# Performance work log

Hardware: AMD Instinct MI355X
Metric: run time of the kernel (lower is better)

## Reference

```python
import jax, jax.numpy as jnp
import numpy as np

B, S, H, I, E, TOPK = 2, 2048, 1024, 2048, 8, 2


def setup_inputs() -> dict:
    key = jax.random.key(0)
    ks = jax.random.split(key, 6)
    return {
        "x": jax.random.normal(ks[0], (B, S, H), dtype=jnp.float32),
        "expert_indices": jax.random.randint(ks[1], (B, S, TOPK), 0, E, dtype=jnp.int64),
        "expert_weights": jax.random.uniform(ks[2], (B, S, TOPK), dtype=jnp.float32),
        "gate_proj": jax.random.normal(ks[3], (E, I, H), dtype=jnp.float32) * 0.02,
        "up_proj": jax.random.normal(ks[4], (E, I, H), dtype=jnp.float32) * 0.02,
        "down_proj": jax.random.normal(ks[5], (E, H, I), dtype=jnp.float32) * 0.02,
    }


def reference(x, expert_indices, expert_weights, gate_proj, up_proj, down_proj):
    # x: [B,S,H]; expert_indices/weights: [B,S,K]; gate/up: [E,I,H]; down: [E,H,I]
    b, s, h = x.shape
    e = gate_proj.shape[0]
    xf = x.reshape(-1, h)                      # [T,H]
    t = xf.shape[0]
    idx = expert_indices.reshape(t, -1)        # [T,K]
    w = expert_weights.reshape(t, -1)          # [T,K]
    # Combine per-(token,slot) weights into a per-(token,expert) weight matrix.
    # Identical math to the per-expert index_add_ in the torch module.
    we = jnp.zeros((t, e), dtype=x.dtype).at[jnp.arange(t)[:, None], idx].add(w)  # [T,E]
    gate = jax.nn.silu(jnp.einsum('th,eih->tei', xf, gate_proj))  # [T,E,I]
    up = jnp.einsum('th,eih->tei', xf, up_proj)                   # [T,E,I]
    out_e = jnp.einsum('tei,ehi->teh', gate * up, down_proj)      # [T,E,H]
    out = jnp.einsum('te,teh->th', we, out_e)                     # [T,H]
    return out.reshape(b, s, h)
```

## Files before the change

kernel.cpp:

```cpp
#include <hip/hip_runtime.h>


#define H_DIM 1024
#define I_DIM 2048
#define N_EXP 8
#define N_TOK 4096
#define N_ENT 8192
#define CAP   9216

typedef __attribute__((ext_vector_type(8))) short bhalf8;
typedef __attribute__((ext_vector_type(4))) float floatx4;

__device__ __forceinline__ unsigned short f2bf(float f) {
  unsigned int u = __float_as_uint(f);
  u += 0x7fffu + ((u >> 16) & 1u);
  return (unsigned short)(u >> 16);
}

__device__ __forceinline__ unsigned int pkbf(float a, float b) {
  unsigned int ua = __float_as_uint(a) + 0x8000u;
  unsigned int ub = __float_as_uint(b) + 0x8000u;
  return __builtin_amdgcn_perm(ub, ua, 0x07060302u);
}

__device__ __forceinline__ void ld16(const void* g, void* l) {
  __builtin_amdgcn_global_load_lds(
      (const __attribute__((address_space(1))) unsigned int*)g,
      (__attribute__((address_space(3))) unsigned int*)l, 16, 0, 0);
}

__global__ __launch_bounds__(256) void prep_kernel(
    const float* __restrict__ x, unsigned short* __restrict__ xb,
    const int* __restrict__ idx, const float* __restrict__ wts,
    int* __restrict__ perm, float* __restrict__ pw, int* __restrict__ inv,
    int* __restrict__ counts, int* __restrict__ poff)
{
  __shared__ int cnt[N_EXP], cur[N_EXP], off[N_EXP];
  const int t = threadIdx.x;
  if (blockIdx.x < (N_TOK * H_DIM) / (256 * 8)) {
    size_t i = ((size_t)blockIdx.x * 256 + t) * 8;
    const float4* sp = (const float4*)(x + i);
    float4 a = sp[0], b = sp[1];
    bhalf8 o;
    o[0] = (short)f2bf(a.x); o[1] = (short)f2bf(a.y); o[2] = (short)f2bf(a.z); o[3] = (short)f2bf(a.w);
    o[4] = (short)f2bf(b.x); o[5] = (short)f2bf(b.y); o[6] = (short)f2bf(b.z); o[7] = (short)f2bf(b.w);
    *(bhalf8*)(xb + i) = o;
    return;
  }
  if (t < N_EXP) { cnt[t] = 0; cur[t] = 0; }
  __syncthreads();
  for (int i = t; i < N_ENT; i += 256) atomicAdd(&cnt[idx[i] & 7], 1);
  __syncthreads();
  if (t == 0) {
    int o = 0;
    for (int e = 0; e < N_EXP; e++) {
      off[e] = o; counts[e] = cnt[e]; poff[e] = o;
      o += ((cnt[e] + 127) >> 7) << 7;
    }
  }
  __syncthreads();
  for (int i = t; i < N_ENT; i += 256) {
    int e = idx[i] & 7;
    int p = atomicAdd(&cur[e], 1);
    int pos = off[e] + p;
    perm[pos] = i >> 1;
    pw[pos] = wts[i];
    inv[i] = pos;
  }
}

__global__ __launch_bounds__(512, 4) void gemm1_kernel(
    const unsigned short* __restrict__ xb,
    const float* __restrict__ gw,
    const float* __restrict__ uw,
    const int* __restrict__ perm,
    const int* __restrict__ counts,
    const int* __restrict__ poff,
    unsigned short* __restrict__ act)
{
  const int e = blockIdx.z;
  const int Ne = counts[e];
  const int mt = blockIdx.y;
  if (mt * 256 >= Ne) return;
  const int NeR = ((Ne + 127) >> 7) << 7;
  const int base = poff[e];
  const int n0 = blockIdx.x * 64;

  __shared__ __align__(16) unsigned short As[256 * 64];
  __shared__ __align__(16) unsigned short Bgs[64 * 64];
  __shared__ __align__(16) unsigned short Bus[64 * 64];

  const int tid = threadIdx.x;
  const int lane = tid & 63;
  const int w = tid >> 6;
  const int wmi = w >> 1;
  const int wnj = w & 1;
  const int i3 = lane >> 3, i7 = lane & 7;
  const int swc = (i7 ^ i3) * 8;

  const unsigned short* pA[4]; unsigned short* lA[4];
#pragma unroll
  for (int t = 0; t < 4; t++) {
    int rloc = w * 32 + t * 8 + i3;
    int rr = mt * 256 + rloc; rr = rr < Ne ? rr : Ne - 1;
    pA[t] = xb + (size_t)perm[base + rr] * H_DIM + swc;
    lA[t] = &As[(w * 32 + t * 8) * 64];
  }
  const int nlocB = w * 8 + i3;
  const size_t wb = (size_t)e * (I_DIM * H_DIM) + (size_t)(n0 + nlocB) * H_DIM + i7 * 8;
  const float* pg = gw + wb;
  const float* pu = uw + wb;
  unsigned short* lBg = &Bgs[nlocB * 64 + ((i7 ^ i3) * 8)];
  unsigned short* lBu = &Bus[nlocB * 64 + ((i7 ^ i3) * 8)];

  floatx4 zero = {0.f, 0.f, 0.f, 0.f};
  floatx4 accg[4][2], accu[4][2];
#pragma unroll
  for (int i = 0; i < 4; i++)
#pragma unroll
    for (int j = 0; j < 2; j++) { accg[i][j] = zero; accu[i][j] = zero; }

  const int quad = lane >> 4, lm = lane & 15;
  const int s7 = lm & 7;

  float4 g0 = *(const float4*)(pg);
  float4 g1 = *(const float4*)(pg + 4);
  float4 u0 = *(const float4*)(pu);
  float4 u1 = *(const float4*)(pu + 4);

  for (int k0 = 0; k0 < H_DIM; k0 += 64) {
    __syncthreads();
#pragma unroll
    for (int t = 0; t < 4; t++) ld16(pA[t] + k0, lA[t]);
    *(uint4*)lBg = make_uint4(pkbf(g0.x, g0.y), pkbf(g0.z, g0.w),
                              pkbf(g1.x, g1.y), pkbf(g1.z, g1.w));
    *(uint4*)lBu = make_uint4(pkbf(u0.x, u0.y), pkbf(u0.z, u0.w),
                              pkbf(u1.x, u1.y), pkbf(u1.z, u1.w));
    __syncthreads();
    if (k0 + 64 < H_DIM) {
      g0 = *(const float4*)(pg + k0 + 64);
      g1 = *(const float4*)(pg + k0 + 68);
      u0 = *(const float4*)(pu + k0 + 64);
      u1 = *(const float4*)(pu + k0 + 68);
    }
#pragma unroll
    for (int kk = 0; kk < 2; kk++) {
      const int kq = kk * 4 + quad;
      const int ko = (kq ^ s7) * 8;
      bhalf8 a[4], bg[2], bu[2];
#pragma unroll
      for (int i = 0; i < 4; i++)
        a[i] = *(const bhalf8*)&As[(wmi * 64 + i * 16 + lm) * 64 + ko];
#pragma unroll
      for (int j = 0; j < 2; j++) {
        bg[j] = *(const bhalf8*)&Bgs[(wnj * 32 + j * 16 + lm) * 64 + ko];
        bu[j] = *(const bhalf8*)&Bus[(wnj * 32 + j * 16 + lm) * 64 + ko];
      }
#pragma unroll
      for (int i = 0; i < 4; i++)
#pragma unroll
        for (int j = 0; j < 2; j++) {
          accg[i][j] = __builtin_amdgcn_mfma_f32_16x16x32_bf16(a[i], bg[j], accg[i][j], 0, 0, 0);
          accu[i][j] = __builtin_amdgcn_mfma_f32_16x16x32_bf16(a[i], bu[j], accu[i][j], 0, 0, 0);
        }
    }
  }

#pragma unroll
  for (int i = 0; i < 4; i++) {
#pragma unroll
    for (int r = 0; r < 4; r++) {
      int row = mt * 256 + wmi * 64 + i * 16 + quad * 4 + r;
      if (row < NeR) {
        size_t rowoff = (size_t)(base + row) * I_DIM;
#pragma unroll
        for (int j = 0; j < 2; j++) {
          int col = n0 + wnj * 32 + j * 16 + lm;
          float g = accg[i][j][r];
          float u = accu[i][j][r];
          float h = (g / (1.f + __expf(-g))) * u;
          act[rowoff + col] = (unsigned short)f2bf(h);
        }
      }
    }
  }
}

__global__ __launch_bounds__(512, 4) void gemm2_kernel(
    const unsigned short* __restrict__ act,
    const float* __restrict__ dw,
    const float* __restrict__ pw,
    const int* __restrict__ counts,
    const int* __restrict__ poff,
    float* __restrict__ ent)
{
  const int e = blockIdx.z;
  const int Ne = counts[e];
  const int mt = blockIdx.y;
  if (mt * 256 >= Ne) return;
  const int NeR = ((Ne + 127) >> 7) << 7;
  const int base = poff[e];
  const int n0 = (blockIdx.x & 7) * 128;
  const int k_lo = (blockIdx.x >> 3) * (I_DIM / 2);

  __shared__ __align__(16) unsigned short As[256 * 64];
  __shared__ __align__(16) unsigned short Bs[128 * 64];

  const int tid = threadIdx.x;
  const int lane = tid & 63;
  const int w = tid >> 6;
  const int wmi = w >> 1, wnj = w & 1;
  const int i3 = lane >> 3, i7 = lane & 7;
  const int swc = (i7 ^ i3) * 8;

  const unsigned short* pA[4]; unsigned short* lA[4];
#pragma unroll
  for (int t = 0; t < 4; t++) {
    int rloc = w * 32 + t * 8 + i3;
    int rr = mt * 256 + rloc; rr = rr < NeR ? rr : NeR - 1;
    pA[t] = act + (size_t)(base + rr) * I_DIM + k_lo + swc;
    lA[t] = &As[(w * 32 + t * 8) * 64];
  }
  const float* pB[2]; unsigned short* lB[2];
#pragma unroll
  for (int t = 0; t < 2; t++) {
    int rloc = w * 16 + t * 8 + i3;
    pB[t] = dw + (size_t)e * (H_DIM * I_DIM) + (size_t)(n0 + rloc) * I_DIM + k_lo + i7 * 8;
    lB[t] = &Bs[rloc * 64 + ((i7 ^ i3) * 8)];
  }

  floatx4 zero = {0.f, 0.f, 0.f, 0.f};
  floatx4 acc[4][4];
#pragma unroll
  for (int i = 0; i < 4; i++)
#pragma unroll
    for (int j = 0; j < 4; j++) acc[i][j] = zero;

  const int quad = lane >> 4, lm = lane & 15;
  const int s7 = lm & 7;

  float4 b00 = *(const float4*)(pB[0]);
  float4 b01 = *(const float4*)(pB[0] + 4);
  float4 b10 = *(const float4*)(pB[1]);
  float4 b11 = *(const float4*)(pB[1] + 4);

  for (int k0 = 0; k0 < I_DIM / 2; k0 += 64) {
    __syncthreads();
#pragma unroll
    for (int t = 0; t < 4; t++) ld16(pA[t] + k0, lA[t]);
    *(uint4*)lB[0] = make_uint4(pkbf(b00.x, b00.y), pkbf(b00.z, b00.w),
                                pkbf(b01.x, b01.y), pkbf(b01.z, b01.w));
    *(uint4*)lB[1] = make_uint4(pkbf(b10.x, b10.y), pkbf(b10.z, b10.w),
                                pkbf(b11.x, b11.y), pkbf(b11.z, b11.w));
    __syncthreads();
    if (k0 + 64 < I_DIM / 2) {
      b00 = *(const float4*)(pB[0] + k0 + 64);
      b01 = *(const float4*)(pB[0] + k0 + 68);
      b10 = *(const float4*)(pB[1] + k0 + 64);
      b11 = *(const float4*)(pB[1] + k0 + 68);
    }
#pragma unroll
    for (int kk = 0; kk < 2; kk++) {
      const int kq = kk * 4 + quad;
      const int ko = (kq ^ s7) * 8;
      bhalf8 a[4], b[4];
#pragma unroll
      for (int i = 0; i < 4; i++)
        a[i] = *(const bhalf8*)&As[(wmi * 64 + i * 16 + lm) * 64 + ko];
#pragma unroll
      for (int j = 0; j < 4; j++)
        b[j] = *(const bhalf8*)&Bs[(wnj * 64 + j * 16 + lm) * 64 + ko];
#pragma unroll
      for (int i = 0; i < 4; i++)
#pragma unroll
        for (int j = 0; j < 4; j++)
          acc[i][j] = __builtin_amdgcn_mfma_f32_16x16x32_bf16(a[i], b[j], acc[i][j], 0, 0, 0);
    }
  }

  float* enth = ent + (size_t)(blockIdx.x >> 3) * CAP * H_DIM;
#pragma unroll
  for (int i = 0; i < 4; i++) {
#pragma unroll
    for (int r = 0; r < 4; r++) {
      int row = mt * 256 + wmi * 64 + i * 16 + quad * 4 + r;
      if (row < Ne) {
        float wt = pw[base + row];
        float* orow = enth + (size_t)(base + row) * H_DIM;
#pragma unroll
        for (int j = 0; j < 4; j++) {
          int col = n0 + wnj * 64 + j * 16 + lm;
          orow[col] = wt * acc[i][j][r];
        }
      }
    }
  }
}

__global__ __launch_bounds__(256) void combine_kernel(
    const float* __restrict__ ent, const int* __restrict__ inv,
    float* __restrict__ out)
{
  const int t = blockIdx.x;
  const int p0 = inv[2 * t], p1 = inv[2 * t + 1];
  const float4* r0 = (const float4*)(ent + (size_t)p0 * H_DIM);
  const float4* r1 = (const float4*)(ent + (size_t)p1 * H_DIM);
  const float4* r2 = (const float4*)(ent + (size_t)(CAP + p0) * H_DIM);
  const float4* r3 = (const float4*)(ent + (size_t)(CAP + p1) * H_DIM);
  float4 a = r0[threadIdx.x], b = r1[threadIdx.x];
  float4 c = r2[threadIdx.x], d = r3[threadIdx.x];
  float4 o = {a.x + b.x + c.x + d.x, a.y + b.y + c.y + d.y,
              a.z + b.z + c.z + d.z, a.w + b.w + c.w + d.w};
  ((float4*)(out + (size_t)t * H_DIM))[threadIdx.x] = o;
}

extern "C" void kernel_launch(void* const* d_in, const int* in_sizes, int n_in,
                              void* d_out, int out_size, void* d_ws, size_t ws_size,
                              hipStream_t stream) {
  const float* x    = (const float*)d_in[0];
  const int*   idx  = (const int*)d_in[1];
  const float* wts  = (const float*)d_in[2];
  const float* gate = (const float*)d_in[3];
  const float* up   = (const float*)d_in[4];
  const float* down = (const float*)d_in[5];
  float* out = (float*)d_out;
  char* ws = (char*)d_ws;

  float*          ent = (float*)(ws + 0);
  unsigned short* act = (unsigned short*)(ws + 75497472);
  unsigned short* xb  = (unsigned short*)(ws + 113246208);
  int*   perm   = (int*)(ws + 121634816);
  float* pw     = (float*)(ws + 121671680);
  int*   inv    = (int*)(ws + 121708544);
  int*   counts = (int*)(ws + 121741312);
  int*   poff   = (int*)(ws + 121741376);

  prep_kernel<<<(N_TOK * H_DIM) / (256 * 8) + 1, 256, 0, stream>>>(
      x, xb, idx, wts, perm, pw, inv, counts, poff);

  gemm1_kernel<<<dim3(I_DIM / 64, 32, N_EXP), 512, 0, stream>>>(
      xb, gate, up, perm, counts, poff, act);

  gemm2_kernel<<<dim3(16, 32, N_EXP), 512, 0, stream>>>(
      act, down, pw, counts, poff, ent);

  combine_kernel<<<N_TOK, 256, 0, stream>>>(ent, inv, out);
}
```

Measured before the change: 383.9 us.

## Fuse combine into down-projection via atomic scatter-add into zeroed output

The output is zeroed inside the prep kernel. The down-projection GEMM then atomically adds weighted results directly into each token's output row using perm. This removes the large per-entry intermediate buffer, the inverse index array and the separate combine kernel. It relies on float atomics, which add L2 atomic traffic and make summation order nondeterministic.

```diff
diff --git a/kernel.cpp b/kernel.cpp
--- a/kernel.cpp
+++ b/kernel.cpp
@@ -31,8 +31,9 @@
 
 __global__ __launch_bounds__(256) void prep_kernel(
     const float* __restrict__ x, unsigned short* __restrict__ xb,
+    float* __restrict__ out,
     const int* __restrict__ idx, const float* __restrict__ wts,
-    int* __restrict__ perm, float* __restrict__ pw, int* __restrict__ inv,
+    int* __restrict__ perm, float* __restrict__ pw,
     int* __restrict__ counts, int* __restrict__ poff)
 {
   __shared__ int cnt[N_EXP], cur[N_EXP], off[N_EXP];
@@ -45,6 +46,10 @@
     o[0] = (short)f2bf(a.x); o[1] = (short)f2bf(a.y); o[2] = (short)f2bf(a.z); o[3] = (short)f2bf(a.w);
     o[4] = (short)f2bf(b.x); o[5] = (short)f2bf(b.y); o[6] = (short)f2bf(b.z); o[7] = (short)f2bf(b.w);
     *(bhalf8*)(xb + i) = o;
+    float4 z4 = {0.f, 0.f, 0.f, 0.f};
+    float4* op = (float4*)(out + (size_t)blockIdx.x * 2048);
+    op[t] = z4;
+    op[t + 256] = z4;
     return;
   }
   if (t < N_EXP) { cnt[t] = 0; cur[t] = 0; }
@@ -65,7 +70,6 @@
     int pos = off[e] + p;
     perm[pos] = i >> 1;
     pw[pos] = wts[i];
-    inv[i] = pos;
   }
 }
 
@@ -190,9 +194,10 @@
     const unsigned short* __restrict__ act,
     const float* __restrict__ dw,
     const float* __restrict__ pw,
+    const int* __restrict__ perm,
     const int* __restrict__ counts,
     const int* __restrict__ poff,
-    float* __restrict__ ent)
+    float* __restrict__ out)
 {
   const int e = blockIdx.z;
   const int Ne = counts[e];
@@ -278,7 +283,6 @@
     }
   }
 
-  float* enth = ent + (size_t)(blockIdx.x >> 3) * CAP * H_DIM;
 #pragma unroll
   for (int i = 0; i < 4; i++) {
 #pragma unroll
@@ -286,32 +290,15 @@
       int row = mt * 256 + wmi * 64 + i * 16 + quad * 4 + r;
       if (row < Ne) {
         float wt = pw[base + row];
-        float* orow = enth + (size_t)(base + row) * H_DIM;
+        float* orow = out + (size_t)perm[base + row] * H_DIM;
 #pragma unroll
         for (int j = 0; j < 4; j++) {
           int col = n0 + wnj * 64 + j * 16 + lm;
-          orow[col] = wt * acc[i][j][r];
+          atomicAdd(&orow[col], wt * acc[i][j][r]);
         }
       }
     }
   }
-}
-
-__global__ __launch_bounds__(256) void combine_kernel(
-    const float* __restrict__ ent, const int* __restrict__ inv,
-    float* __restrict__ out)
-{
-  const int t = blockIdx.x;
-  const int p0 = inv[2 * t], p1 = inv[2 * t + 1];
-  const float4* r0 = (const float4*)(ent + (size_t)p0 * H_DIM);
-  const float4* r1 = (const float4*)(ent + (size_t)p1 * H_DIM);
-  const float4* r2 = (const float4*)(ent + (size_t)(CAP + p0) * H_DIM);
-  const float4* r3 = (const float4*)(ent + (size_t)(CAP + p1) * H_DIM);
-  float4 a = r0[threadIdx.x], b = r1[threadIdx.x];
-  float4 c = r2[threadIdx.x], d = r3[threadIdx.x];
-  float4 o = {a.x + b.x + c.x + d.x, a.y + b.y + c.y + d.y,
-              a.z + b.z + c.z + d.z, a.w + b.w + c.w + d.w};
-  ((float4*)(out + (size_t)t * H_DIM))[threadIdx.x] = o;
 }
 
 extern "C" void kernel_launch(void* const* d_in, const int* in_sizes, int n_in,
@@ -326,23 +313,19 @@
   float* out = (float*)d_out;
   char* ws = (char*)d_ws;
 
-  float*          ent = (float*)(ws + 0);
-  unsigned short* act = (unsigned short*)(ws + 75497472);
-  unsigned short* xb  = (unsigned short*)(ws + 113246208);
-  int*   perm   = (int*)(ws + 121634816);
-  float* pw     = (float*)(ws + 121671680);
-  int*   inv    = (int*)(ws + 121708544);
-  int*   counts = (int*)(ws + 121741312);
-  int*   poff   = (int*)(ws + 121741376);
+  unsigned short* act = (unsigned short*)(ws + 0);
+  unsigned short* xb  = (unsigned short*)(ws + 37748736);
+  int*   perm   = (int*)(ws + 46137344);
+  float* pw     = (float*)(ws + 46174208);
+  int*   counts = (int*)(ws + 46211072);
+  int*   poff   = (int*)(ws + 46211136);
 
   prep_kernel<<<(N_TOK * H_DIM) / (256 * 8) + 1, 256, 0, stream>>>(
-      x, xb, idx, wts, perm, pw, inv, counts, poff);
+      x, xb, out, idx, wts, perm, pw, counts, poff);
 
   gemm1_kernel<<<dim3(I_DIM / 64, 32, N_EXP), 512, 0, stream>>>(
       xb, gate, up, perm, counts, poff, act);
 
   gemm2_kernel<<<dim3(16, 32, N_EXP), 512, 0, stream>>>(
-      act, down, pw, counts, poff, ent);
-
-  combine_kernel<<<N_TOK, 256, 0, stream>>>(ent, inv, out);
-}
+      act, down, pw, perm, counts, poff, out);
+}
```

Result: slower. 409.3 us (+6.6%).

## Double-buffer LDS tiles in both expert GEMM kernels to overlap loads with MFMA

Applied to the files above, without the earlier changes.

Both grouped GEMM kernels now keep two LDS buffers for the A and B tiles and alternate between them. The next K-slice is staged while the current one is computed, so each step needs one barrier instead of two. This is meant to hide global-load and LDS-write latency behind MFMA work. It doubles LDS use per block and lowers the occupancy hint in launch bounds from 4 to 2 blocks per CU, which can reduce latency hiding from concurrent blocks.

```diff
diff --git a/kernel.cpp b/kernel.cpp
--- a/kernel.cpp
+++ b/kernel.cpp
@@ -69,7 +69,44 @@
   }
 }
 
-__global__ __launch_bounds__(512, 4) void gemm1_kernel(
+#define G1_STAGE_A(ASX, KOFF)                                               \
+  _Pragma("unroll")                                                         \
+  for (int t_ = 0; t_ < 4; t_++) ld16(pA[t_] + (KOFF), &ASX[lAo[t_]]);
+
+#define G1_LOAD_B(KOFF)                                                     \
+  g0 = *(const float4*)(pg + (KOFF));  g1 = *(const float4*)(pg + (KOFF) + 4); \
+  u0 = *(const float4*)(pu + (KOFF));  u1 = *(const float4*)(pu + (KOFF) + 4);
+
+#define G1_WRITE_B(BGX, BUX)                                                \
+  *(uint4*)&BGX[bo] = make_uint4(pkbf(g0.x, g0.y), pkbf(g0.z, g0.w),        \
+                                 pkbf(g1.x, g1.y), pkbf(g1.z, g1.w));       \
+  *(uint4*)&BUX[bo] = make_uint4(pkbf(u0.x, u0.y), pkbf(u0.z, u0.w),        \
+                                 pkbf(u1.x, u1.y), pkbf(u1.z, u1.w));
+
+#define G1_COMPUTE(ASX, BGX, BUX)                                           \
+  _Pragma("unroll")                                                         \
+  for (int kk = 0; kk < 2; kk++) {                                          \
+    const int kq = kk * 4 + quad;                                           \
+    const int ko = (kq ^ s7) * 8;                                           \
+    bhalf8 a_[4], bg_[2], bu_[2];                                           \
+    _Pragma("unroll")                                                       \
+    for (int i = 0; i < 4; i++)                                             \
+      a_[i] = *(const bhalf8*)&ASX[(wmi * 64 + i * 16 + lm) * 64 + ko];     \
+    _Pragma("unroll")                                                       \
+    for (int j = 0; j < 2; j++) {                                           \
+      bg_[j] = *(const bhalf8*)&BGX[(wnj * 32 + j * 16 + lm) * 64 + ko];    \
+      bu_[j] = *(const bhalf8*)&BUX[(wnj * 32 + j * 16 + lm) * 64 + ko];    \
+    }                                                                       \
+    _Pragma("unroll")                                                       \
+    for (int i = 0; i < 4; i++)                                             \
+      _Pragma("unroll")                                                     \
+      for (int j = 0; j < 2; j++) {                                         \
+        accg[i][j] = __builtin_amdgcn_mfma_f32_16x16x32_bf16(a_[i], bg_[j], accg[i][j], 0, 0, 0); \
+        accu[i][j] = __builtin_amdgcn_mfma_f32_16x16x32_bf16(a_[i], bu_[j], accu[i][j], 0, 0, 0); \
+      }                                                                     \
+  }
+
+__global__ __launch_bounds__(512, 2) void gemm1_kernel(
     const unsigned short* __restrict__ xb,
     const float* __restrict__ gw,
     const float* __restrict__ uw,
@@ -86,9 +123,12 @@
   const int base = poff[e];
   const int n0 = blockIdx.x * 64;
 
-  __shared__ __align__(16) unsigned short As[256 * 64];
-  __shared__ __align__(16) unsigned short Bgs[64 * 64];
-  __shared__ __align__(16) unsigned short Bus[64 * 64];
+  __shared__ __align__(16) unsigned short As0[256 * 64];
+  __shared__ __align__(16) unsigned short As1[256 * 64];
+  __shared__ __align__(16) unsigned short Bg0[64 * 64];
+  __shared__ __align__(16) unsigned short Bg1[64 * 64];
+  __shared__ __align__(16) unsigned short Bu0[64 * 64];
+  __shared__ __align__(16) unsigned short Bu1[64 * 64];
 
   const int tid = threadIdx.x;
   const int lane = tid & 63;
@@ -98,20 +138,19 @@
   const int i3 = lane >> 3, i7 = lane & 7;
   const int swc = (i7 ^ i3) * 8;
 
-  const unsigned short* pA[4]; unsigned short* lA[4];
+  const unsigned short* pA[4]; int lAo[4];
 #pragma unroll
   for (int t = 0; t < 4; t++) {
     int rloc = w * 32 + t * 8 + i3;
     int rr = mt * 256 + rloc; rr = rr < Ne ? rr : Ne - 1;
     pA[t] = xb + (size_t)perm[base + rr] * H_DIM + swc;
-    lA[t] = &As[(w * 32 + t * 8) * 64];
+    lAo[t] = (w * 32 + t * 8) * 64;
   }
   const int nlocB = w * 8 + i3;
   const size_t wb = (size_t)e * (I_DIM * H_DIM) + (size_t)(n0 + nlocB) * H_DIM + i7 * 8;
   const float* pg = gw + wb;
   const float* pu = uw + wb;
-  unsigned short* lBg = &Bgs[nlocB * 64 + ((i7 ^ i3) * 8)];
-  unsigned short* lBu = &Bus[nlocB * 64 + ((i7 ^ i3) * 8)];
+  const int bo = nlocB * 64 + ((i7 ^ i3) * 8);
 
   floatx4 zero = {0.f, 0.f, 0.f, 0.f};
   floatx4 accg[4][2], accu[4][2];
@@ -123,48 +162,31 @@
   const int quad = lane >> 4, lm = lane & 15;
   const int s7 = lm & 7;
 
-  float4 g0 = *(const float4*)(pg);
-  float4 g1 = *(const float4*)(pg + 4);
-  float4 u0 = *(const float4*)(pu);
-  float4 u1 = *(const float4*)(pu + 4);
-
-  for (int k0 = 0; k0 < H_DIM; k0 += 64) {
+  float4 g0, g1, u0, u1;
+
+  G1_STAGE_A(As0, 0);
+  G1_LOAD_B(0);
+  G1_WRITE_B(Bg0, Bu0);
+  __syncthreads();
+
+  for (int k0 = 0; k0 < H_DIM - 128; k0 += 128) {
+    G1_STAGE_A(As1, k0 + 64);
+    G1_LOAD_B(k0 + 64);
+    G1_COMPUTE(As0, Bg0, Bu0);
+    G1_WRITE_B(Bg1, Bu1);
     __syncthreads();
-#pragma unroll
-    for (int t = 0; t < 4; t++) ld16(pA[t] + k0, lA[t]);
-    *(uint4*)lBg = make_uint4(pkbf(g0.x, g0.y), pkbf(g0.z, g0.w),
-                              pkbf(g1.x, g1.y), pkbf(g1.z, g1.w));
-    *(uint4*)lBu = make_uint4(pkbf(u0.x, u0.y), pkbf(u0.z, u0.w),
-                              pkbf(u1.x, u1.y), pkbf(u1.z, u1.w));
+    G1_STAGE_A(As0, k0 + 128);
+    G1_LOAD_B(k0 + 128);
+    G1_COMPUTE(As1, Bg1, Bu1);
+    G1_WRITE_B(Bg0, Bu0);
     __syncthreads();
-    if (k0 + 64 < H_DIM) {
-      g0 = *(const float4*)(pg + k0 + 64);
-      g1 = *(const float4*)(pg + k0 + 68);
-      u0 = *(const float4*)(pu + k0 + 64);
-      u1 = *(const float4*)(pu + k0 + 68);
-    }
-#pragma unroll
-    for (int kk = 0; kk < 2; kk++) {
-      const int kq = kk * 4 + quad;
-      const int ko = (kq ^ s7) * 8;
-      bhalf8 a[4], bg[2], bu[2];
-#pragma unroll
-      for (int i = 0; i < 4; i++)
-        a[i] = *(const bhalf8*)&As[(wmi * 64 + i * 16 + lm) * 64 + ko];
-#pragma unroll
-      for (int j = 0; j < 2; j++) {
-        bg[j] = *(const bhalf8*)&Bgs[(wnj * 32 + j * 16 + lm) * 64 + ko];
-        bu[j] = *(const bhalf8*)&Bus[(wnj * 32 + j * 16 + lm) * 64 + ko];
-      }
-#pragma unroll
-      for (int i = 0; i < 4; i++)
-#pragma unroll
-        for (int j = 0; j < 2; j++) {
-          accg[i][j] = __builtin_amdgcn_mfma_f32_16x16x32_bf16(a[i], bg[j], accg[i][j], 0, 0, 0);
-          accu[i][j] = __builtin_amdgcn_mfma_f32_16x16x32_bf16(a[i], bu[j], accu[i][j], 0, 0, 0);
-        }
-    }
-  }
+  }
+  G1_STAGE_A(As1, H_DIM - 64);
+  G1_LOAD_B(H_DIM - 64);
+  G1_COMPUTE(As0, Bg0, Bu0);
+  G1_WRITE_B(Bg1, Bu1);
+  __syncthreads();
+  G1_COMPUTE(As1, Bg1, Bu1);
 
 #pragma unroll
   for (int i = 0; i < 4; i++) {
@@ -186,7 +208,40 @@
   }
 }
 
-__global__ __launch_bounds__(512, 4) void gemm2_kernel(
+#define G2_STAGE_A(ASX, KOFF)                                               \
+  _Pragma("unroll")                                                         \
+  for (int t_ = 0; t_ < 4; t_++) ld16(pA[t_] + (KOFF), &ASX[lAo[t_]]);
+
+#define G2_LOAD_B(KOFF)                                                     \
+  b00 = *(const float4*)(pB[0] + (KOFF)); b01 = *(const float4*)(pB[0] + (KOFF) + 4); \
+  b10 = *(const float4*)(pB[1] + (KOFF)); b11 = *(const float4*)(pB[1] + (KOFF) + 4);
+
+#define G2_WRITE_B(BSX)                                                     \
+  *(uint4*)&BSX[boB[0]] = make_uint4(pkbf(b00.x, b00.y), pkbf(b00.z, b00.w),\
+                                     pkbf(b01.x, b01.y), pkbf(b01.z, b01.w));\
+  *(uint4*)&BSX[boB[1]] = make_uint4(pkbf(b10.x, b10.y), pkbf(b10.z, b10.w),\
+                                     pkbf(b11.x, b11.y), pkbf(b11.z, b11.w));
+
+#define G2_COMPUTE(ASX, BSX)                                                \
+  _Pragma("unroll")                                                         \
+  for (int kk = 0; kk < 2; kk++) {                                          \
+    const int kq = kk * 4 + quad;                                           \
+    const int ko = (kq ^ s7) * 8;                                           \
+    bhalf8 a_[4], b_[4];                                                    \
+    _Pragma("unroll")                                                       \
+    for (int i = 0; i < 4; i++)                                             \
+      a_[i] = *(const bhalf8*)&ASX[(wmi * 64 + i * 16 + lm) * 64 + ko];     \
+    _Pragma("unroll")                                                       \
+    for (int j = 0; j < 4; j++)                                             \
+      b_[j] = *(const bhalf8*)&BSX[(wnj * 64 + j * 16 + lm) * 64 + ko];     \
+    _Pragma("unroll")                                                       \
+    for (int i = 0; i < 4; i++)                                             \
+      _Pragma("unroll")                                                     \
+      for (int j = 0; j < 4; j++)                                           \
+        acc[i][j] = __builtin_amdgcn_mfma_f32_16x16x32_bf16(a_[i], b_[j], acc[i][j], 0, 0, 0); \
+  }
+
+__global__ __launch_bounds__(512, 2) void gemm2_kernel(
     const unsigned short* __restrict__ act,
     const float* __restrict__ dw,
     const float* __restrict__ pw,
@@ -202,9 +257,12 @@
   const int base = poff[e];
   const int n0 = (blockIdx.x & 7) * 128;
   const int k_lo = (blockIdx.x >> 3) * (I_DIM / 2);
-
-  __shared__ __align__(16) unsigned short As[256 * 64];
-  __shared__ __align__(16) unsigned short Bs[128 * 64];
+  const int KLEN = I_DIM / 2;
+
+  __shared__ __align__(16) unsigned short As0[256 * 64];
+  __shared__ __align__(16) unsigned short As1[256 * 64];
+  __shared__ __align__(16) unsigned short Bs0[128 * 64];
+  __shared__ __align__(16) unsigned short Bs1[128 * 64];
 
   const int tid = threadIdx.x;
   const int lane = tid & 63;
@@ -213,20 +271,20 @@
   const int i3 = lane >> 3, i7 = lane & 7;
   const int swc = (i7 ^ i3) * 8;
 
-  const unsigned short* pA[4]; unsigned short* lA[4];
+  const unsigned short* pA[4]; int lAo[4];
 #pragma unroll
   for (int t = 0; t < 4; t++) {
     int rloc = w * 32 + t * 8 + i3;
     int rr = mt * 256 + rloc; rr = rr < NeR ? rr : NeR - 1;
     pA[t] = act + (size_t)(base + rr) * I_DIM + k_lo + swc;
-    lA[t] = &As[(w * 32 + t * 8) * 64];
-  }
-  const float* pB[2]; unsigned short* lB[2];
+    lAo[t] = (w * 32 + t * 8) * 64;
+  }
+  const float* pB[2]; int boB[2];
 #pragma unroll
   for (int t = 0; t < 2; t++) {
     int rloc = w * 16 + t * 8 + i3;
     pB[t] = dw + (size_t)e * (H_DIM * I_DIM) + (size_t)(n0 + rloc) * I_DIM + k_lo + i7 * 8;
-    lB[t] = &Bs[rloc * 64 + ((i7 ^ i3) * 8)];
+    boB[t] = rloc * 64 + ((i7 ^ i3) * 8);
   }
 
   floatx4 zero = {0.f, 0.f, 0.f, 0.f};
@@ -239,44 +297,31 @@
   const int quad = lane >> 4, lm = lane & 15;
   const int s7 = lm & 7;
 
-  float4 b00 = *(const float4*)(pB[0]);
-  float4 b01 = *(const float4*)(pB[0] + 4);
-  float4 b10 = *(const float4*)(pB[1]);
-  float4 b11 = *(const float4*)(pB[1] + 4);
-
-  for (int k0 = 0; k0 < I_DIM / 2; k0 += 64) {
+  float4 b00, b01, b10, b11;
+
+  G2_STAGE_A(As0, 0);
+  G2_LOAD_B(0);
+  G2_WRITE_B(Bs0);
+  __syncthreads();
+
+  for (int k0 = 0; k0 < KLEN - 128; k0 += 128) {
+    G2_STAGE_A(As1, k0 + 64);
+    G2_LOAD_B(k0 + 64);
+    G2_COMPUTE(As0, Bs0);
+    G2_WRITE_B(Bs1);
     __syncthreads();
-#pragma unroll
-    for (int t = 0; t < 4; t++) ld16(pA[t] + k0, lA[t]);
-    *(uint4*)lB[0] = make_uint4(pkbf(b00.x, b00.y), pkbf(b00.z, b00.w),
-                                pkbf(b01.x, b01.y), pkbf(b01.z, b01.w));
-    *(uint4*)lB[1] = make_uint4(pkbf(b10.x, b10.y), pkbf(b10.z, b10.w),
-                                pkbf(b11.x, b11.y), pkbf(b11.z, b11.w));
+    G2_STAGE_A(As0, k0 + 128);
+    G2_LOAD_B(k0 + 128);
+    G2_COMPUTE(As1, Bs1);
+    G2_WRITE_B(Bs0);
     __syncthreads();
-    if (k0 + 64 < I_DIM / 2) {
-      b00 = *(const float4*)(pB[0] + k0 + 64);
-      b01 = *(const float4*)(pB[0] + k0 + 68);
-      b10 = *(const float4*)(pB[1] + k0 + 64);
-      b11 = *(const float4*)(pB[1] + k0 + 68);
-    }
-#pragma unroll
-    for (int kk = 0; kk < 2; kk++) {
-      const int kq = kk * 4 + quad;
-      const int ko = (kq ^ s7) * 8;
-      bhalf8 a[4], b[4];
-#pragma unroll
-      for (int i = 0; i < 4; i++)
-        a[i] = *(const bhalf8*)&As[(wmi * 64 + i * 16 + lm) * 64 + ko];
-#pragma unroll
-      for (int j = 0; j < 4; j++)
-        b[j] = *(const bhalf8*)&Bs[(wnj * 64 + j * 16 + lm) * 64 + ko];
-#pragma unroll
-      for (int i = 0; i < 4; i++)
-#pragma unroll
-        for (int j = 0; j < 4; j++)
-          acc[i][j] = __builtin_amdgcn_mfma_f32_16x16x32_bf16(a[i], b[j], acc[i][j], 0, 0, 0);
-    }
-  }
+  }
+  G2_STAGE_A(As1, KLEN - 64);
+  G2_LOAD_B(KLEN - 64);
+  G2_COMPUTE(As0, Bs0);
+  G2_WRITE_B(Bs1);
+  __syncthreads();
+  G2_COMPUTE(As1, Bs1);
 
   float* enth = ent + (size_t)(blockIdx.x >> 3) * CAP * H_DIM;
 #pragma unroll
```

Result: slower. 459.1 us (+19.6%).
